# Performance work log

Hardware: AMD Instinct MI355X
Metric: run time of the kernel (lower is better)

The kernel has to match this reference:

```python
import jax, jax.numpy as jnp
import numpy as np

TAU = 0.5
EPS = 1e-08
NORM_EPS = 1e-12  # F.normalize clamp

BS = 4096
D = 256


def _l2_normalize(x):
    n = jnp.linalg.norm(x, axis=1, keepdims=True)
    return x / jnp.maximum(n, NORM_EPS)


def setup_inputs() -> dict:
    key = jax.random.key(0)
    k1, k2 = jax.random.split(key)
    zi = jax.random.normal(k1, (BS, D), dtype=jnp.float32)
    zj = jax.random.normal(k2, (BS, D), dtype=jnp.float32)
    return {"zi": zi, "zj": zj}


def reference(zi, zj):
    bs = zi.shape[0]
    zi_n = _l2_normalize(zi)
    zj_n = _l2_normalize(zj)
    z = jnp.concatenate([zi_n, zj_n], axis=0)  # [2bs, d]
    # cosine sim of unit vectors == dot product
    sim = (z @ z.T) / TAU  # [2bs, 2bs]
    # positive pairs: (i, i+bs) and (i+bs, i) -> same diag values twice
    pos_diag = jnp.sum(zi_n * zj_n, axis=1) / TAU  # [bs]
    sim_pos = jnp.exp(jnp.concatenate([pos_diag, pos_diag]))  # [2bs]
    # negatives: all off-diagonal entries per row
    exp_sim = jnp.exp(sim)
    neg_sum = jnp.sum(exp_sim, axis=1) - jnp.diagonal(exp_sim)  # [2bs]
    loss = jnp.mean(-jnp.log(sim_pos / (neg_sum + EPS)))
    return loss
```

## Files before the change

### kernel.cpp

```cpp
#include <hip/hip_runtime.h>

#define N_TOT 8192
#define BSZ   4096
#define DIM   256

typedef __attribute__((ext_vector_type(8))) short bf16x8;
typedef __attribute__((ext_vector_type(4))) float f32x4;

#define PRESCALE 1.69864362f

__device__ __forceinline__ unsigned short f2bf(float f) {
    unsigned int u = __builtin_bit_cast(unsigned int, f);
    u = (u + 0x7fffu + ((u >> 16) & 1u)) >> 16;
    return (unsigned short)u;
}

__device__ __forceinline__ void async_copy16(const void* g, void* l) {
    __builtin_amdgcn_global_load_lds((const __attribute__((address_space(1))) void*)g,
                                     (__attribute__((address_space(3))) void*)l,
                                     16, 0, 0);
}

__global__ __launch_bounds__(256) void norm_kernel(const float* __restrict__ zi,
                                                   const float* __restrict__ zj,
                                                   unsigned short* __restrict__ zb,
                                                   float* __restrict__ posPart) {
    __shared__ float buf[2][256];
    const int wid  = threadIdx.x >> 6;
    const int lane = threadIdx.x & 63;
    const int pair = blockIdx.x * 2 + (wid & 1);
    const bool isZj = (wid >= 2);
    const float* src = isZj ? (zj + (size_t)pair * DIM) : (zi + (size_t)pair * DIM);
    float4 v = ((const float4*)src)[lane];
    float ss = v.x * v.x + v.y * v.y + v.z * v.z + v.w * v.w;
    #pragma unroll
    for (int off = 1; off < 64; off <<= 1) ss += __shfl_xor(ss, off);
    float inv = 1.0f / fmaxf(sqrtf(ss), 1e-12f);
    float4 nv = make_float4(v.x * inv, v.y * inv, v.z * inv, v.w * inv);

    const int outRow = isZj ? (pair + BSZ) : pair;
    ushort4 o;
    o.x = f2bf(nv.x * PRESCALE); o.y = f2bf(nv.y * PRESCALE);
    o.z = f2bf(nv.z * PRESCALE); o.w = f2bf(nv.w * PRESCALE);
    ((ushort4*)(zb + (size_t)outRow * DIM))[lane] = o;

    if (!isZj) ((float4*)&buf[wid & 1][0])[lane] = nv;
    __syncthreads();
    if (isZj) {
        float4 a = ((float4*)&buf[wid & 1][0])[lane];
        float d = a.x * nv.x + a.y * nv.y + a.z * nv.z + a.w * nv.w;
        #pragma unroll
        for (int off = 1; off < 64; off <<= 1) d += __shfl_xor(d, off);
        if (lane == 0) posPart[pair] = d;
    }
}

__global__ __launch_bounds__(256, 4) void sim_kernel(const unsigned short* __restrict__ zb,
                                                     float* __restrict__ partial) {
    __shared__ alignas(16) char smem[32768];

    const int t    = threadIdx.x;
    const int lane = t & 63;
    const int wid  = t >> 6;
    const int wr   = wid >> 1;
    const int wc   = wid & 1;

    const int k = blockIdx.x;
    int bi = (int)((129.0f - sqrtf(16641.0f - 8.0f * (float)k)) * 0.5f);
    while (bi * 64 - bi * (bi - 1) / 2 > k) bi--;
    while ((bi + 1) * 64 - (bi + 1) * bi / 2 <= k) bi++;
    const int bj = bi + (k - (bi * 64 - bi * (bi - 1) / 2));
    const bool diag = (bi == bj);

    const int row0 = bi * 128;
    const int col0 = bj * 128;

    f32x4 acc[4][4];
    #pragma unroll
    for (int m = 0; m < 4; m++)
        #pragma unroll
        for (int n = 0; n < 4; n++) acc[m][n] = (f32x4){0.f, 0.f, 0.f, 0.f};

    #define STAGE(b, kt) do {                                                   \
        _Pragma("unroll")                                                       \
        for (int i = 0; i < 2; i++) {                                           \
            const int s   = i * 256 + t;           \
            const int pr_ = s >> 3;                           \
            const int c_  = (s & 7) ^ (pr_ & 7);                                \
            const int r_  = pr_ * 2 + (c_ >> 2);           \
            const int q_  = c_ & 3;                            \
            char* ldsbase = smem + (b) * 16384 + (i * 256 + wid * 64) * 16;     \
            async_copy16(zb + (size_t)(row0 + r_) * DIM + (kt) * 32 + q_ * 8,   \
                         ldsbase);                                              \
            async_copy16(zb + (size_t)(col0 + r_) * DIM + (kt) * 32 + q_ * 8,   \
                         ldsbase + 8192);                                       \
        } } while (0)

    STAGE(0, 0);

    #pragma unroll
    for (int kt = 0; kt < 8; ++kt) {
        const int cur = kt & 1;
        if (kt < 7) {
            STAGE(cur ^ 1, kt + 1);
            asm volatile("s_waitcnt vmcnt(4)" ::: "memory");
        } else {
            asm volatile("s_waitcnt vmcnt(0)" ::: "memory");
        }
        __builtin_amdgcn_sched_barrier(0);
        __builtin_amdgcn_s_barrier();

        const char* Ab = smem + cur * 16384;
        const char* Bb = Ab + 8192;
        const int q = lane >> 4;
        bf16x8 af[4], bfr[4];
        #pragma unroll
        for (int m = 0; m < 4; m++) {
            const int rr  = wr * 64 + m * 16 + (lane & 15);
            const int pr_ = rr >> 1;
            const int sl_ = (((rr & 1) << 2) | q) ^ (pr_ & 7);
            af[m] = *(const bf16x8*)(Ab + pr_ * 128 + sl_ * 16);
        }
        #pragma unroll
        for (int n = 0; n < 4; n++) {
            const int rr  = wc * 64 + n * 16 + (lane & 15);
            const int pr_ = rr >> 1;
            const int sl_ = (((rr & 1) << 2) | q) ^ (pr_ & 7);
            bfr[n] = *(const bf16x8*)(Bb + pr_ * 128 + sl_ * 16);
        }
        #pragma unroll
        for (int m = 0; m < 4; m++)
            #pragma unroll
            for (int n = 0; n < 4; n++)
                acc[m][n] = __builtin_amdgcn_mfma_f32_16x16x32_bf16(af[m], bfr[n], acc[m][n], 0, 0, 0);

        __builtin_amdgcn_sched_barrier(0);
        __builtin_amdgcn_s_barrier();
    }
    #undef STAGE

    float rsum[4][4];
    float csum[4];
    #pragma unroll
    for (int m = 0; m < 4; m++)
        #pragma unroll
        for (int j = 0; j < 4; j++) rsum[m][j] = 0.f;
    #pragma unroll
    for (int n = 0; n < 4; n++) csum[n] = 0.f;

    const int g       = lane >> 4;
    const int c15     = lane & 15;
    const int colbase = col0 + wc * 64 + c15;
    const int rowbase = row0 + wr * 64 + (g << 2);
    #pragma unroll
    for (int m = 0; m < 4; m++) {
        #pragma unroll
        for (int n = 0; n < 4; n++) {
            const int colg = colbase + n * 16;
            #pragma unroll
            for (int j = 0; j < 4; j++) {
                const int rowg = rowbase + m * 16 + j;
                float e = exp2f(acc[m][n][j]);
                if (diag && rowg == colg) e = 0.0f;
                rsum[m][j] += e;
                csum[n] += e;
            }
        }
    }

    if (!diag) {
        #pragma unroll
        for (int n = 0; n < 4; n++) {
            float s = csum[n];
            s += __shfl_xor(s, 16);
            s += __shfl_xor(s, 32);
            csum[n] = s;
        }
        if (lane < 16) {
            float* dst = partial + (size_t)(bi * 2 + wr) * N_TOT;
            #pragma unroll
            for (int n = 0; n < 4; n++)
                dst[colbase + n * 16] = csum[n];
        }
    }

    float* sw = (float*)smem + wid * 1280;
    #pragma unroll
    for (int m = 0; m < 4; m++)
        #pragma unroll
        for (int j = 0; j < 4; j++)
            sw[(m * 16 + (g << 2) + j) * 20 + c15] = rsum[m][j];

    f32x4 v0 = *(const f32x4*)(sw + lane * 20 + 0);
    f32x4 v1 = *(const f32x4*)(sw + lane * 20 + 4);
    f32x4 v2 = *(const f32x4*)(sw + lane * 20 + 8);
    f32x4 v3 = *(const f32x4*)(sw + lane * 20 + 12);
    float tot = (v0[0] + v0[1] + v0[2] + v0[3]) + (v1[0] + v1[1] + v1[2] + v1[3])
              + (v2[0] + v2[1] + v2[2] + v2[3]) + (v3[0] + v3[1] + v3[2] + v3[3]);
    partial[(size_t)(bj * 2 + wc) * N_TOT + row0 + wr * 64 + lane] = tot;
}

__global__ __launch_bounds__(256) void rowlog_kernel(const float* __restrict__ partial,
                                                     float* __restrict__ logPart) {
    const int lane = threadIdx.x & 63;
    const int w    = threadIdx.x >> 6;
    const int row  = blockIdx.x * 64 + lane;
    float s = 0.f;
    #pragma unroll 8
    for (int p = w * 32; p < w * 32 + 32; p++) s += partial[(size_t)p * N_TOT + row];
    __shared__ float red[4][64];
    red[w][lane] = s;
    __syncthreads();
    if (w == 0) {
        float tot = red[0][lane] + red[1][lane] + red[2][lane] + red[3][lane];
        float v = logf(tot + 1e-8f);
        #pragma unroll
        for (int off = 1; off < 64; off <<= 1) v += __shfl_xor(v, off);
        if (lane == 0) logPart[blockIdx.x] = v;
    }
}

__global__ __launch_bounds__(256) void final_kernel(const float* __restrict__ logPart,
                                                    const float* __restrict__ posPart,
                                                    float* __restrict__ out) {
    const int t = threadIdx.x;
    float ps = 0.f;
    for (int i = t; i < BSZ; i += 256) ps += posPart[i];
    float ls = (t < 128) ? logPart[t] : 0.f;
    #pragma unroll
    for (int off = 1; off < 64; off <<= 1) {
        ps += __shfl_xor(ps, off);
        ls += __shfl_xor(ls, off);
    }
    __shared__ float redp[4], redl[4];
    const int lane = t & 63, wid = t >> 6;
    if (lane == 0) { redp[wid] = ps; redl[wid] = ls; }
    __syncthreads();
    if (t == 0) {
        const float posSum = redp[0] + redp[1] + redp[2] + redp[3];
        const float logSum = redl[0] + redl[1] + redl[2] + redl[3];
        out[0] = logSum / (float)N_TOT - 2.0f * posSum / (float)BSZ;
    }
}

extern "C" void kernel_launch(void* const* d_in, const int* in_sizes, int n_in,
                              void* d_out, int out_size, void* d_ws, size_t ws_size,
                              hipStream_t stream) {
    const float* zi = (const float*)d_in[0];
    const float* zj = (const float*)d_in[1];
    float* out = (float*)d_out;

    char* ws = (char*)d_ws;
    unsigned short* zb = (unsigned short*)ws;
    float* partial     = (float*)(ws + (size_t)(4 << 20));
    float* logPart     = (float*)(ws + (size_t)(8 << 20));
    float* posPart     = (float*)(ws + (size_t)(8 << 20) + 4096);

    norm_kernel<<<2048, 256, 0, stream>>>(zi, zj, zb, posPart);
    sim_kernel<<<2080, 256, 0, stream>>>(zb, partial);
    rowlog_kernel<<<128, 256, 0, stream>>>(partial, logPart);
    final_kernel<<<1, 256, 0, stream>>>(logPart, posPart, out);
}
```

Measured before the change: 45.03 us.

## Enlarge sim tiles to 256x256 with 8 waves, block swizzle and split MFMA phases

The similarity kernel now has each 512-thread block compute a 256x256 tile of the upper-triangular block grid instead of 128x128, so each staged row is reused across more output. Block indices are swizzled to change tile order across compute units. Each k-step is split into two MFMA halves with raised wave priority, and the next stage is issued before the current one's math. The aim is to cut global/LDS traffic per FLOP and the block scheduling overhead, at the cost of more registers, 64 KB LDS, fewer blocks (528) and more wasted work on diagonal tiles.

```diff
diff --git a/kernel.cpp b/kernel.cpp
--- a/kernel.cpp
+++ b/kernel.cpp
@@ -55,105 +55,123 @@
     }
 }
 
-__global__ __launch_bounds__(256, 4) void sim_kernel(const unsigned short* __restrict__ zb,
+__global__ __launch_bounds__(512, 2) void sim_kernel(const unsigned short* __restrict__ zb,
                                                      float* __restrict__ partial) {
-    __shared__ alignas(16) char smem[32768];
+    __shared__ alignas(16) char smem[65536];
 
     const int t    = threadIdx.x;
     const int lane = t & 63;
     const int wid  = t >> 6;
-    const int wr   = wid >> 1;
-    const int wc   = wid & 1;
-
-    const int k = blockIdx.x;
-    int bi = (int)((129.0f - sqrtf(16641.0f - 8.0f * (float)k)) * 0.5f);
-    while (bi * 64 - bi * (bi - 1) / 2 > k) bi--;
-    while ((bi + 1) * 64 - (bi + 1) * bi / 2 <= k) bi++;
-    const int bj = bi + (k - (bi * 64 - bi * (bi - 1) / 2));
+    const int wr   = wid >> 2;
+    const int wc   = wid & 3;
+    const int g    = lane >> 4;
+    const int c15  = lane & 15;
+
+    const int orig = blockIdx.x;
+    const int swz  = (orig & 7) * 66 + (orig >> 3);
+    int bi = (int)((65.0f - sqrtf(4225.0f - 8.0f * (float)swz)) * 0.5f);
+    while (bi * 32 - bi * (bi - 1) / 2 > swz) bi--;
+    while ((bi + 1) * 32 - (bi + 1) * bi / 2 <= swz) bi++;
+    const int bj = bi + (swz - (bi * 32 - bi * (bi - 1) / 2));
     const bool diag = (bi == bj);
 
-    const int row0 = bi * 128;
-    const int col0 = bj * 128;
-
-    f32x4 acc[4][4];
-    #pragma unroll
-    for (int m = 0; m < 4; m++)
+    const int row0 = bi * 256;
+    const int col0 = bj * 256;
+
+    f32x4 acc[8][4];
+    #pragma unroll
+    for (int m = 0; m < 8; m++)
         #pragma unroll
         for (int n = 0; n < 4; n++) acc[m][n] = (f32x4){0.f, 0.f, 0.f, 0.f};
 
     #define STAGE(b, kt) do {                                                   \
         _Pragma("unroll")                                                       \
         for (int i = 0; i < 2; i++) {                                           \
-            const int s   = i * 256 + t;           \
-            const int pr_ = s >> 3;                           \
-            const int c_  = (s & 7) ^ (pr_ & 7);                                \
-            const int r_  = pr_ * 2 + (c_ >> 2);           \
-            const int q_  = c_ & 3;                            \
-            char* ldsbase = smem + (b) * 16384 + (i * 256 + wid * 64) * 16;     \
+            const int e_  = i * 512 + t;                                        \
+            const int pr_ = e_ >> 3;                                            \
+            const int c_  = (e_ & 7) ^ (pr_ & 7);                               \
+            const int r_  = pr_ * 2 + (c_ >> 2);                                \
+            const int q_  = c_ & 3;                                             \
+            char* ldsbase = smem + (b) * 32768 + (i * 512 + wid * 64) * 16;     \
             async_copy16(zb + (size_t)(row0 + r_) * DIM + (kt) * 32 + q_ * 8,   \
                          ldsbase);                                              \
             async_copy16(zb + (size_t)(col0 + r_) * DIM + (kt) * 32 + q_ * 8,   \
-                         ldsbase + 8192);                                       \
+                         ldsbase + 16384);                                      \
         } } while (0)
 
     STAGE(0, 0);
+    STAGE(1, 1);
+    asm volatile("s_waitcnt vmcnt(4)" ::: "memory");
+    __builtin_amdgcn_s_barrier();
 
     #pragma unroll
     for (int kt = 0; kt < 8; ++kt) {
         const int cur = kt & 1;
-        if (kt < 7) {
-            STAGE(cur ^ 1, kt + 1);
-            asm volatile("s_waitcnt vmcnt(4)" ::: "memory");
-        } else {
-            asm volatile("s_waitcnt vmcnt(0)" ::: "memory");
-        }
-        __builtin_amdgcn_sched_barrier(0);
-        __builtin_amdgcn_s_barrier();
-
-        const char* Ab = smem + cur * 16384;
-        const char* Bb = Ab + 8192;
-        const int q = lane >> 4;
-        bf16x8 af[4], bfr[4];
+        const char* Ab = smem + cur * 32768;
+        const char* Bb = Ab + 16384;
+        const int q = g;
+
+        if (kt < 7) STAGE(cur ^ 1, kt + 1);
+        bf16x8 bfr[4], af[4];
+        #pragma unroll
+        for (int n = 0; n < 4; n++) {
+            const int rr  = wc * 64 + n * 16 + c15;
+            const int pr_ = rr >> 1;
+            const int sl_ = (((rr & 1) << 2) | q) ^ (pr_ & 7);
+            bfr[n] = *(const bf16x8*)(Bb + pr_ * 128 + sl_ * 16);
+        }
         #pragma unroll
         for (int m = 0; m < 4; m++) {
-            const int rr  = wr * 64 + m * 16 + (lane & 15);
+            const int rr  = wr * 128 + m * 16 + c15;
             const int pr_ = rr >> 1;
             const int sl_ = (((rr & 1) << 2) | q) ^ (pr_ & 7);
             af[m] = *(const bf16x8*)(Ab + pr_ * 128 + sl_ * 16);
         }
-        #pragma unroll
-        for (int n = 0; n < 4; n++) {
-            const int rr  = wc * 64 + n * 16 + (lane & 15);
+        __builtin_amdgcn_sched_barrier(0);
+        __builtin_amdgcn_s_setprio(1);
+        #pragma unroll
+        for (int m = 0; m < 4; m++)
+            #pragma unroll
+            for (int n = 0; n < 4; n++)
+                acc[m][n] = __builtin_amdgcn_mfma_f32_16x16x32_bf16(af[m], bfr[n], acc[m][n], 0, 0, 0);
+        __builtin_amdgcn_s_setprio(0);
+        __builtin_amdgcn_sched_barrier(0);
+        __builtin_amdgcn_s_barrier();
+
+        #pragma unroll
+        for (int m = 0; m < 4; m++) {
+            const int rr  = wr * 128 + (m + 4) * 16 + c15;
             const int pr_ = rr >> 1;
             const int sl_ = (((rr & 1) << 2) | q) ^ (pr_ & 7);
-            bfr[n] = *(const bf16x8*)(Bb + pr_ * 128 + sl_ * 16);
-        }
+            af[m] = *(const bf16x8*)(Ab + pr_ * 128 + sl_ * 16);
+        }
+        __builtin_amdgcn_sched_barrier(0);
+        __builtin_amdgcn_s_setprio(1);
         #pragma unroll
         for (int m = 0; m < 4; m++)
             #pragma unroll
             for (int n = 0; n < 4; n++)
-                acc[m][n] = __builtin_amdgcn_mfma_f32_16x16x32_bf16(af[m], bfr[n], acc[m][n], 0, 0, 0);
-
-        __builtin_amdgcn_sched_barrier(0);
+                acc[m + 4][n] = __builtin_amdgcn_mfma_f32_16x16x32_bf16(af[m], bfr[n], acc[m + 4][n], 0, 0, 0);
+        __builtin_amdgcn_s_setprio(0);
+        __builtin_amdgcn_sched_barrier(0);
+        if (kt < 7) asm volatile("s_waitcnt vmcnt(0)" ::: "memory");
         __builtin_amdgcn_s_barrier();
     }
     #undef STAGE
 
-    float rsum[4][4];
-    float csum[4];
-    #pragma unroll
-    for (int m = 0; m < 4; m++)
-        #pragma unroll
-        for (int j = 0; j < 4; j++) rsum[m][j] = 0.f;
-    #pragma unroll
-    for (int n = 0; n < 4; n++) csum[n] = 0.f;
-
-    const int g       = lane >> 4;
-    const int c15     = lane & 15;
+    float rsumN[8][4];
+    float csum[4][2];
+    #pragma unroll
+    for (int m = 0; m < 8; m++)
+        #pragma unroll
+        for (int j = 0; j < 4; j++) rsumN[m][j] = 0.f;
+    #pragma unroll
+    for (int n = 0; n < 4; n++) { csum[n][0] = 0.f; csum[n][1] = 0.f; }
+
     const int colbase = col0 + wc * 64 + c15;
-    const int rowbase = row0 + wr * 64 + (g << 2);
-    #pragma unroll
-    for (int m = 0; m < 4; m++) {
+    const int rowbase = row0 + wr * 128 + (g << 2);
+    #pragma unroll
+    for (int m = 0; m < 8; m++) {
         #pragma unroll
         for (int n = 0; n < 4; n++) {
             const int colg = colbase + n * 16;
@@ -162,42 +180,55 @@
                 const int rowg = rowbase + m * 16 + j;
                 float e = exp2f(acc[m][n][j]);
                 if (diag && rowg == colg) e = 0.0f;
-                rsum[m][j] += e;
-                csum[n] += e;
+                rsumN[m][j] += e;
+                csum[n][m >> 2] += e;
             }
         }
     }
 
     if (!diag) {
         #pragma unroll
-        for (int n = 0; n < 4; n++) {
-            float s = csum[n];
-            s += __shfl_xor(s, 16);
-            s += __shfl_xor(s, 32);
-            csum[n] = s;
-        }
+        for (int n = 0; n < 4; n++)
+            #pragma unroll
+            for (int ms = 0; ms < 2; ms++) {
+                float s = csum[n][ms];
+                s += __shfl_xor(s, 16);
+                s += __shfl_xor(s, 32);
+                csum[n][ms] = s;
+            }
         if (lane < 16) {
-            float* dst = partial + (size_t)(bi * 2 + wr) * N_TOT;
-            #pragma unroll
-            for (int n = 0; n < 4; n++)
-                dst[colbase + n * 16] = csum[n];
+            #pragma unroll
+            for (int ms = 0; ms < 2; ms++) {
+                float* dst = partial + (size_t)(bi * 4 + wr * 2 + ms) * N_TOT;
+                #pragma unroll
+                for (int n = 0; n < 4; n++)
+                    dst[colbase + n * 16] = csum[n][ms];
+            }
         }
     }
 
     float* sw = (float*)smem + wid * 1280;
     #pragma unroll
-    for (int m = 0; m < 4; m++)
-        #pragma unroll
-        for (int j = 0; j < 4; j++)
-            sw[(m * 16 + (g << 2) + j) * 20 + c15] = rsum[m][j];
-
-    f32x4 v0 = *(const f32x4*)(sw + lane * 20 + 0);
-    f32x4 v1 = *(const f32x4*)(sw + lane * 20 + 4);
-    f32x4 v2 = *(const f32x4*)(sw + lane * 20 + 8);
-    f32x4 v3 = *(const f32x4*)(sw + lane * 20 + 12);
-    float tot = (v0[0] + v0[1] + v0[2] + v0[3]) + (v1[0] + v1[1] + v1[2] + v1[3])
-              + (v2[0] + v2[1] + v2[2] + v2[3]) + (v3[0] + v3[1] + v3[2] + v3[3]);
-    partial[(size_t)(bj * 2 + wc) * N_TOT + row0 + wr * 64 + lane] = tot;
+    for (int ms = 0; ms < 2; ms++) {
+        if (ms) {
+            asm volatile("s_waitcnt lgkmcnt(0)" ::: "memory");
+            __builtin_amdgcn_sched_barrier(0);
+        }
+        #pragma unroll
+        for (int mq = 0; mq < 4; mq++)
+            #pragma unroll
+            for (int j = 0; j < 4; j++)
+                sw[(mq * 16 + (g << 2) + j) * 20 + c15] = rsumN[ms * 4 + mq][j];
+        asm volatile("s_waitcnt lgkmcnt(0)" ::: "memory");
+        __builtin_amdgcn_sched_barrier(0);
+        f32x4 v0 = *(const f32x4*)(sw + lane * 20 + 0);
+        f32x4 v1 = *(const f32x4*)(sw + lane * 20 + 4);
+        f32x4 v2 = *(const f32x4*)(sw + lane * 20 + 8);
+        f32x4 v3 = *(const f32x4*)(sw + lane * 20 + 12);
+        float tot = (v0[0] + v0[1] + v0[2] + v0[3]) + (v1[0] + v1[1] + v1[2] + v1[3])
+                  + (v2[0] + v2[1] + v2[2] + v2[3]) + (v3[0] + v3[1] + v3[2] + v3[3]);
+        partial[(size_t)(bj * 4 + wc) * N_TOT + row0 + wr * 128 + ms * 64 + lane] = tot;
+    }
 }
 
 __global__ __launch_bounds__(256) void rowlog_kernel(const float* __restrict__ partial,
@@ -257,7 +288,7 @@
     float* posPart     = (float*)(ws + (size_t)(8 << 20) + 4096);
 
     norm_kernel<<<2048, 256, 0, stream>>>(zi, zj, zb, posPart);
-    sim_kernel<<<2080, 256, 0, stream>>>(zb, partial);
+    sim_kernel<<<528, 512, 0, stream>>>(zb, partial);
     rowlog_kernel<<<128, 256, 0, stream>>>(partial, logPart);
     final_kernel<<<1, 256, 0, stream>>>(logPart, posPart, out);
 }
```

Result: slower. 53.29 us (+18.3%).

## Compute two column tiles per block to reuse the row tile in sim kernel

Applied to the files above, without the earlier changes.

Each sim_kernel block now computes two adjacent 128x128 upper-triangular column tiles against one row tile, cutting the grid from 2080 to 1056 blocks. The shared A tile and its LDS fragments are reused across twice the MFMAs. The k-loop is also restructured to a single barrier per iteration, issuing the next stage after the barrier with a full vmcnt wait, and wraps the MFMA block in setprio. This doubles accumulator registers (occupancy hint drops to 2) and LDS to 48KB, and adds odd-tile edge handling that could hurt load balance.

```diff
diff --git a/kernel.cpp b/kernel.cpp
--- a/kernel.cpp
+++ b/kernel.cpp
@@ -55,149 +55,168 @@
     }
 }
 
-__global__ __launch_bounds__(256, 4) void sim_kernel(const unsigned short* __restrict__ zb,
+__global__ __launch_bounds__(256, 2) void sim_kernel(const unsigned short* __restrict__ zb,
                                                      float* __restrict__ partial) {
-    __shared__ alignas(16) char smem[32768];
+    __shared__ alignas(16) char smem[49152];
 
     const int t    = threadIdx.x;
     const int lane = t & 63;
     const int wid  = t >> 6;
     const int wr   = wid >> 1;
     const int wc   = wid & 1;
-
+    const int g    = lane >> 4;
+    const int c15  = lane & 15;
+
+    auto S = [](int b) { int mm = b >> 1; return mm * (65 - mm) + ((b & 1) ? (32 - mm) : 0); };
     const int k = blockIdx.x;
-    int bi = (int)((129.0f - sqrtf(16641.0f - 8.0f * (float)k)) * 0.5f);
-    while (bi * 64 - bi * (bi - 1) / 2 > k) bi--;
-    while ((bi + 1) * 64 - (bi + 1) * bi / 2 <= k) bi++;
-    const int bj = bi + (k - (bi * 64 - bi * (bi - 1) / 2));
-    const bool diag = (bi == bj);
-
+    int bi = 2 * (int)((65.0f - sqrtf(fmaxf(4225.0f - 4.0f * (float)k, 0.f))) * 0.5f);
+    if (bi < 0) bi = 0; if (bi > 63) bi = 63;
+    while (bi > 0 && S(bi) > k) bi--;
+    while (S(bi + 1) <= k) bi++;
+    const int tt   = k - S(bi);
+    const int bj1  = bi + 2 * tt;
+    const bool valid2 = (bj1 + 1) <= 63;
+    const bool diag   = (bi == bj1);
     const int row0 = bi * 128;
-    const int col0 = bj * 128;
-
-    f32x4 acc[4][4];
-    #pragma unroll
-    for (int m = 0; m < 4; m++)
-        #pragma unroll
-        for (int n = 0; n < 4; n++) acc[m][n] = (f32x4){0.f, 0.f, 0.f, 0.f};
+    const int col1 = bj1 * 128;
+    const int col2 = valid2 ? col1 + 128 : col1;
+
+    f32x4 acc[2][4][4];
+    #pragma unroll
+    for (int jj = 0; jj < 2; jj++)
+        #pragma unroll
+        for (int m = 0; m < 4; m++)
+            #pragma unroll
+            for (int n = 0; n < 4; n++) acc[jj][m][n] = (f32x4){0.f, 0.f, 0.f, 0.f};
 
     #define STAGE(b, kt) do {                                                   \
         _Pragma("unroll")                                                       \
         for (int i = 0; i < 2; i++) {                                           \
-            const int s   = i * 256 + t;           \
-            const int pr_ = s >> 3;                           \
-            const int c_  = (s & 7) ^ (pr_ & 7);                                \
-            const int r_  = pr_ * 2 + (c_ >> 2);           \
-            const int q_  = c_ & 3;                            \
-            char* ldsbase = smem + (b) * 16384 + (i * 256 + wid * 64) * 16;     \
-            async_copy16(zb + (size_t)(row0 + r_) * DIM + (kt) * 32 + q_ * 8,   \
-                         ldsbase);                                              \
-            async_copy16(zb + (size_t)(col0 + r_) * DIM + (kt) * 32 + q_ * 8,   \
-                         ldsbase + 8192);                                       \
+            const int e_  = i * 256 + t;                  \
+            const int pr_ = e_ >> 3;                          \
+            const int c_  = (e_ & 7) ^ (pr_ & 7);                               \
+            const int r_  = pr_ * 2 + (c_ >> 2);                                \
+            const int q_  = c_ & 3;                                             \
+            char* lb = smem + (b) * 24576 + (i * 256 + wid * 64) * 16;          \
+            const size_t ko = (size_t)(kt) * 32 + q_ * 8;                       \
+            async_copy16(zb + (size_t)(row0 + r_) * DIM + ko, lb);              \
+            async_copy16(zb + (size_t)(col1 + r_) * DIM + ko, lb + 8192);       \
+            async_copy16(zb + (size_t)(col2 + r_) * DIM + ko, lb + 16384);      \
         } } while (0)
 
     STAGE(0, 0);
 
     #pragma unroll
     for (int kt = 0; kt < 8; ++kt) {
-        const int cur = kt & 1;
-        if (kt < 7) {
-            STAGE(cur ^ 1, kt + 1);
-            asm volatile("s_waitcnt vmcnt(4)" ::: "memory");
-        } else {
-            asm volatile("s_waitcnt vmcnt(0)" ::: "memory");
-        }
+        asm volatile("s_waitcnt vmcnt(0)" ::: "memory");
         __builtin_amdgcn_sched_barrier(0);
         __builtin_amdgcn_s_barrier();
-
-        const char* Ab = smem + cur * 16384;
-        const char* Bb = Ab + 8192;
-        const int q = lane >> 4;
-        bf16x8 af[4], bfr[4];
+        if (kt < 7) STAGE((kt + 1) & 1, kt + 1);
+
+        const char* Ab = smem + (kt & 1) * 24576;
+        bf16x8 af[4], b1[4], b2[4];
         #pragma unroll
         for (int m = 0; m < 4; m++) {
-            const int rr  = wr * 64 + m * 16 + (lane & 15);
-            const int pr_ = rr >> 1;
-            const int sl_ = (((rr & 1) << 2) | q) ^ (pr_ & 7);
-            af[m] = *(const bf16x8*)(Ab + pr_ * 128 + sl_ * 16);
+            const int rr = wr * 64 + m * 16 + c15;
+            const int pr = rr >> 1;
+            const int sl = (((rr & 1) << 2) | g) ^ (pr & 7);
+            af[m] = *(const bf16x8*)(Ab + pr * 128 + sl * 16);
         }
         #pragma unroll
         for (int n = 0; n < 4; n++) {
-            const int rr  = wc * 64 + n * 16 + (lane & 15);
-            const int pr_ = rr >> 1;
-            const int sl_ = (((rr & 1) << 2) | q) ^ (pr_ & 7);
-            bfr[n] = *(const bf16x8*)(Bb + pr_ * 128 + sl_ * 16);
-        }
-        #pragma unroll
-        for (int m = 0; m < 4; m++)
-            #pragma unroll
-            for (int n = 0; n < 4; n++)
-                acc[m][n] = __builtin_amdgcn_mfma_f32_16x16x32_bf16(af[m], bfr[n], acc[m][n], 0, 0, 0);
-
+            const int rr = wc * 64 + n * 16 + c15;
+            const int pr = rr >> 1;
+            const int sl = (((rr & 1) << 2) | g) ^ (pr & 7);
+            b1[n] = *(const bf16x8*)(Ab + 8192  + pr * 128 + sl * 16);
+            b2[n] = *(const bf16x8*)(Ab + 16384 + pr * 128 + sl * 16);
+        }
+        __builtin_amdgcn_s_setprio(1);
+        #pragma unroll
+        for (int m = 0; m < 4; m++)
+            #pragma unroll
+            for (int n = 0; n < 4; n++) {
+                acc[0][m][n] = __builtin_amdgcn_mfma_f32_16x16x32_bf16(af[m], b1[n], acc[0][m][n], 0, 0, 0);
+                acc[1][m][n] = __builtin_amdgcn_mfma_f32_16x16x32_bf16(af[m], b2[n], acc[1][m][n], 0, 0, 0);
+            }
+        __builtin_amdgcn_s_setprio(0);
         __builtin_amdgcn_sched_barrier(0);
-        __builtin_amdgcn_s_barrier();
     }
     #undef STAGE
-
-    float rsum[4][4];
-    float csum[4];
-    #pragma unroll
-    for (int m = 0; m < 4; m++)
-        #pragma unroll
-        for (int j = 0; j < 4; j++) rsum[m][j] = 0.f;
-    #pragma unroll
-    for (int n = 0; n < 4; n++) csum[n] = 0.f;
-
-    const int g       = lane >> 4;
-    const int c15     = lane & 15;
-    const int colbase = col0 + wc * 64 + c15;
+    __builtin_amdgcn_s_barrier();
+
     const int rowbase = row0 + wr * 64 + (g << 2);
-    #pragma unroll
-    for (int m = 0; m < 4; m++) {
-        #pragma unroll
-        for (int n = 0; n < 4; n++) {
-            const int colg = colbase + n * 16;
-            #pragma unroll
-            for (int j = 0; j < 4; j++) {
-                const int rowg = rowbase + m * 16 + j;
-                float e = exp2f(acc[m][n][j]);
-                if (diag && rowg == colg) e = 0.0f;
-                rsum[m][j] += e;
-                csum[n] += e;
-            }
-        }
-    }
-
-    if (!diag) {
-        #pragma unroll
-        for (int n = 0; n < 4; n++) {
-            float s = csum[n];
-            s += __shfl_xor(s, 16);
-            s += __shfl_xor(s, 32);
-            csum[n] = s;
-        }
-        if (lane < 16) {
-            float* dst = partial + (size_t)(bi * 2 + wr) * N_TOT;
-            #pragma unroll
-            for (int n = 0; n < 4; n++)
-                dst[colbase + n * 16] = csum[n];
-        }
-    }
-
     float* sw = (float*)smem + wid * 1280;
-    #pragma unroll
-    for (int m = 0; m < 4; m++)
-        #pragma unroll
-        for (int j = 0; j < 4; j++)
-            sw[(m * 16 + (g << 2) + j) * 20 + c15] = rsum[m][j];
-
-    f32x4 v0 = *(const f32x4*)(sw + lane * 20 + 0);
-    f32x4 v1 = *(const f32x4*)(sw + lane * 20 + 4);
-    f32x4 v2 = *(const f32x4*)(sw + lane * 20 + 8);
-    f32x4 v3 = *(const f32x4*)(sw + lane * 20 + 12);
-    float tot = (v0[0] + v0[1] + v0[2] + v0[3]) + (v1[0] + v1[1] + v1[2] + v1[3])
-              + (v2[0] + v2[1] + v2[2] + v2[3]) + (v3[0] + v3[1] + v3[2] + v3[3]);
-    partial[(size_t)(bj * 2 + wc) * N_TOT + row0 + wr * 64 + lane] = tot;
+
+    #pragma unroll
+    for (int jj = 0; jj < 2; jj++) {
+        const bool active = (jj == 0) || valid2;
+        const bool dg     = (jj == 0) && diag;
+        const int col0j   = jj ? col2 : col1;
+        const int colbase = col0j + wc * 64 + c15;
+
+        float rsum[4][4];
+        float csum[4];
+        #pragma unroll
+        for (int m = 0; m < 4; m++)
+            #pragma unroll
+            for (int j = 0; j < 4; j++) rsum[m][j] = 0.f;
+        #pragma unroll
+        for (int n = 0; n < 4; n++) csum[n] = 0.f;
+
+        #pragma unroll
+        for (int m = 0; m < 4; m++) {
+            #pragma unroll
+            for (int n = 0; n < 4; n++) {
+                const int colg = colbase + n * 16;
+                #pragma unroll
+                for (int j = 0; j < 4; j++) {
+                    const int rowg = rowbase + m * 16 + j;
+                    float e = exp2f(acc[jj][m][n][j]);
+                    if (dg && rowg == colg) e = 0.0f;
+                    rsum[m][j] += e;
+                    csum[n] += e;
+                }
+            }
+        }
+
+        if (!dg) {
+            #pragma unroll
+            for (int n = 0; n < 4; n++) {
+                float s = csum[n];
+                s += __shfl_xor(s, 16);
+                s += __shfl_xor(s, 32);
+                csum[n] = s;
+            }
+            if (active && lane < 16) {
+                float* dst = partial + (size_t)(bi * 2 + wr) * N_TOT;
+                #pragma unroll
+                for (int n = 0; n < 4; n++)
+                    dst[colbase + n * 16] = csum[n];
+            }
+        }
+
+        if (jj) {
+            asm volatile("s_waitcnt lgkmcnt(0)" ::: "memory");
+            __builtin_amdgcn_sched_barrier(0);
+        }
+        #pragma unroll
+        for (int m = 0; m < 4; m++)
+            #pragma unroll
+            for (int j = 0; j < 4; j++)
+                sw[(m * 16 + (g << 2) + j) * 20 + c15] = rsum[m][j];
+        asm volatile("s_waitcnt lgkmcnt(0)" ::: "memory");
+        __builtin_amdgcn_sched_barrier(0);
+        f32x4 v0 = *(const f32x4*)(sw + lane * 20 + 0);
+        f32x4 v1 = *(const f32x4*)(sw + lane * 20 + 4);
+        f32x4 v2 = *(const f32x4*)(sw + lane * 20 + 8);
+        f32x4 v3 = *(const f32x4*)(sw + lane * 20 + 12);
+        float tot = (v0[0] + v0[1] + v0[2] + v0[3]) + (v1[0] + v1[1] + v1[2] + v1[3])
+                  + (v2[0] + v2[1] + v2[2] + v2[3]) + (v3[0] + v3[1] + v3[2] + v3[3]);
+        if (active) {
+            const int bj = bj1 + jj;
+            partial[(size_t)(bj * 2 + wc) * N_TOT + row0 + wr * 64 + lane] = tot;
+        }
+    }
 }
 
 __global__ __launch_bounds__(256) void rowlog_kernel(const float* __restrict__ partial,
@@ -257,7 +276,7 @@
     float* posPart     = (float*)(ws + (size_t)(8 << 20) + 4096);
 
     norm_kernel<<<2048, 256, 0, stream>>>(zi, zj, zb, posPart);
-    sim_kernel<<<2080, 256, 0, stream>>>(zb, partial);
+    sim_kernel<<<1056, 256, 0, stream>>>(zb, partial);
     rowlog_kernel<<<128, 256, 0, stream>>>(partial, logPart);
     final_kernel<<<1, 256, 0, stream>>>(logPart, posPart, out);
 }
```

Result: slower. 49.70 us (+10.4%).

## Switch similarity GEMM operands from bf16 to fp8 with permuted layout

Applied to the files above, without the earlier changes.

The normalized embeddings are now packed as fp8 (e4m3) in a K-permuted order, and the similarity kernel uses fp8 MFMA instructions with half the K-loop iterations and half the bytes staged per tile. This cuts global and LDS traffic and doubles MFMA throughput per byte. The cost is lower precision in the exp of the similarities, which could shift the loss beyond tolerance. An explicit LDS wait is also added before the row-sum readback.

```diff
diff --git a/kernel.cpp b/kernel.cpp
--- a/kernel.cpp
+++ b/kernel.cpp
@@ -4,16 +4,10 @@
 #define BSZ   4096
 #define DIM   256
 
-typedef __attribute__((ext_vector_type(8))) short bf16x8;
 typedef __attribute__((ext_vector_type(4))) float f32x4;
+typedef __attribute__((ext_vector_type(2))) unsigned long long u64x2;
 
 #define PRESCALE 1.69864362f
-
-__device__ __forceinline__ unsigned short f2bf(float f) {
-    unsigned int u = __builtin_bit_cast(unsigned int, f);
-    u = (u + 0x7fffu + ((u >> 16) & 1u)) >> 16;
-    return (unsigned short)u;
-}
 
 __device__ __forceinline__ void async_copy16(const void* g, void* l) {
     __builtin_amdgcn_global_load_lds((const __attribute__((address_space(1))) void*)g,
@@ -23,7 +17,7 @@
 
 __global__ __launch_bounds__(256) void norm_kernel(const float* __restrict__ zi,
                                                    const float* __restrict__ zj,
-                                                   unsigned short* __restrict__ zb,
+                                                   unsigned char* __restrict__ zb,
                                                    float* __restrict__ posPart) {
     __shared__ float buf[2][256];
     const int wid  = threadIdx.x >> 6;
@@ -39,10 +33,12 @@
     float4 nv = make_float4(v.x * inv, v.y * inv, v.z * inv, v.w * inv);
 
     const int outRow = isZj ? (pair + BSZ) : pair;
-    ushort4 o;
-    o.x = f2bf(nv.x * PRESCALE); o.y = f2bf(nv.y * PRESCALE);
-    o.z = f2bf(nv.z * PRESCALE); o.w = f2bf(nv.w * PRESCALE);
-    ((ushort4*)(zb + (size_t)outRow * DIM))[lane] = o;
+    const int j8  = lane >> 1;
+    const int off4 = ((j8 >> 3) << 6) + ((j8 & 3) << 4) + (((j8 >> 2) & 1) << 3)
+                   + ((lane & 1) << 2);
+    int pk = __builtin_amdgcn_cvt_pk_fp8_f32(nv.x * PRESCALE, nv.y * PRESCALE, 0, false);
+    pk     = __builtin_amdgcn_cvt_pk_fp8_f32(nv.z * PRESCALE, nv.w * PRESCALE, pk, true);
+    *(int*)(zb + (size_t)outRow * 256 + off4) = pk;
 
     if (!isZj) ((float4*)&buf[wid & 1][0])[lane] = nv;
     __syncthreads();
@@ -55,7 +51,7 @@
     }
 }
 
-__global__ __launch_bounds__(256, 4) void sim_kernel(const unsigned short* __restrict__ zb,
+__global__ __launch_bounds__(256, 4) void sim_kernel(const unsigned char* __restrict__ zb,
                                                      float* __restrict__ partial) {
     __shared__ alignas(16) char smem[32768];
 
@@ -64,6 +60,8 @@
     const int wid  = t >> 6;
     const int wr   = wid >> 1;
     const int wc   = wid & 1;
+    const int g    = lane >> 4;
+    const int c15  = lane & 15;
 
     const int k = blockIdx.x;
     int bi = (int)((129.0f - sqrtf(16641.0f - 8.0f * (float)k)) * 0.5f);
@@ -84,24 +82,23 @@
     #define STAGE(b, kt) do {                                                   \
         _Pragma("unroll")                                                       \
         for (int i = 0; i < 2; i++) {                                           \
-            const int s   = i * 256 + t;           \
-            const int pr_ = s >> 3;                           \
-            const int c_  = (s & 7) ^ (pr_ & 7);                                \
-            const int r_  = pr_ * 2 + (c_ >> 2);           \
-            const int q_  = c_ & 3;                            \
-            char* ldsbase = smem + (b) * 16384 + (i * 256 + wid * 64) * 16;     \
-            async_copy16(zb + (size_t)(row0 + r_) * DIM + (kt) * 32 + q_ * 8,   \
-                         ldsbase);                                              \
-            async_copy16(zb + (size_t)(col0 + r_) * DIM + (kt) * 32 + q_ * 8,   \
-                         ldsbase + 8192);                                       \
+            const int e_  = i * 256 + t;                   \
+            const int rr_ = e_ >> 2;                       \
+            const int p_  = e_ & 3;                             \
+            const int g_  = p_ ^ ((rr_ >> 1) & 3);           \
+            char* lb = smem + (b) * 16384 + (i * 256 + wid * 64) * 16;          \
+            async_copy16(zb + (size_t)(row0 + rr_) * 256 + (kt) * 64 + g_ * 16, \
+                         lb);                                                   \
+            async_copy16(zb + (size_t)(col0 + rr_) * 256 + (kt) * 64 + g_ * 16, \
+                         lb + 8192);                                            \
         } } while (0)
 
     STAGE(0, 0);
 
     #pragma unroll
-    for (int kt = 0; kt < 8; ++kt) {
+    for (int kt = 0; kt < 4; ++kt) {
         const int cur = kt & 1;
-        if (kt < 7) {
+        if (kt < 3) {
             STAGE(cur ^ 1, kt + 1);
             asm volatile("s_waitcnt vmcnt(4)" ::: "memory");
         } else {
@@ -112,27 +109,28 @@
 
         const char* Ab = smem + cur * 16384;
         const char* Bb = Ab + 8192;
-        const int q = lane >> 4;
-        bf16x8 af[4], bfr[4];
+        u64x2 af[4], bfr[4];
         #pragma unroll
         for (int m = 0; m < 4; m++) {
-            const int rr  = wr * 64 + m * 16 + (lane & 15);
-            const int pr_ = rr >> 1;
-            const int sl_ = (((rr & 1) << 2) | q) ^ (pr_ & 7);
-            af[m] = *(const bf16x8*)(Ab + pr_ * 128 + sl_ * 16);
+            const int rr = wr * 64 + m * 16 + c15;
+            const int p  = g ^ ((rr >> 1) & 3);
+            af[m] = *(const u64x2*)(Ab + rr * 64 + p * 16);
         }
         #pragma unroll
         for (int n = 0; n < 4; n++) {
-            const int rr  = wc * 64 + n * 16 + (lane & 15);
-            const int pr_ = rr >> 1;
-            const int sl_ = (((rr & 1) << 2) | q) ^ (pr_ & 7);
-            bfr[n] = *(const bf16x8*)(Bb + pr_ * 128 + sl_ * 16);
+            const int rr = wc * 64 + n * 16 + c15;
+            const int p  = g ^ ((rr >> 1) & 3);
+            bfr[n] = *(const u64x2*)(Bb + rr * 64 + p * 16);
         }
         #pragma unroll
         for (int m = 0; m < 4; m++)
             #pragma unroll
-            for (int n = 0; n < 4; n++)
-                acc[m][n] = __builtin_amdgcn_mfma_f32_16x16x32_bf16(af[m], bfr[n], acc[m][n], 0, 0, 0);
+            for (int n = 0; n < 4; n++) {
+                acc[m][n] = __builtin_amdgcn_mfma_f32_16x16x32_fp8_fp8(
+                    (long)af[m].x, (long)bfr[n].x, acc[m][n], 0, 0, 0);
+                acc[m][n] = __builtin_amdgcn_mfma_f32_16x16x32_fp8_fp8(
+                    (long)af[m].y, (long)bfr[n].y, acc[m][n], 0, 0, 0);
+            }
 
         __builtin_amdgcn_sched_barrier(0);
         __builtin_amdgcn_s_barrier();
@@ -148,8 +146,6 @@
     #pragma unroll
     for (int n = 0; n < 4; n++) csum[n] = 0.f;
 
-    const int g       = lane >> 4;
-    const int c15     = lane & 15;
     const int colbase = col0 + wc * 64 + c15;
     const int rowbase = row0 + wr * 64 + (g << 2);
     #pragma unroll
@@ -190,7 +186,8 @@
         #pragma unroll
         for (int j = 0; j < 4; j++)
             sw[(m * 16 + (g << 2) + j) * 20 + c15] = rsum[m][j];
-
+    asm volatile("s_waitcnt lgkmcnt(0)" ::: "memory");
+    __builtin_amdgcn_sched_barrier(0);
     f32x4 v0 = *(const f32x4*)(sw + lane * 20 + 0);
     f32x4 v1 = *(const f32x4*)(sw + lane * 20 + 4);
     f32x4 v2 = *(const f32x4*)(sw + lane * 20 + 8);
@@ -251,7 +248,7 @@
     float* out = (float*)d_out;
 
     char* ws = (char*)d_ws;
-    unsigned short* zb = (unsigned short*)ws;
+    unsigned char* zb = (unsigned char*)ws;
     float* partial     = (float*)(ws + (size_t)(4 << 20));
     float* logPart     = (float*)(ws + (size_t)(8 << 20));
     float* posPart     = (float*)(ws + (size_t)(8 << 20) + 4096);
```

New measurement: 38.57 us. -14.4%, faster.
